# Kernel optimization log

Measured on AMD Instinct MI355X. Metric: run time of the kernel, lower is better.

## Reference

```python
import jax, jax.numpy as jnp
import numpy as np

H = 128          # hidden_size
EF = 2           # expansion_factor
E = H * EF       # expanded hidden size
K = 4            # conv kernel size
R = 8            # dt_rank = ceil(128/16)
L = 2            # num_layers
BATCH = 2
SEQ = 1024
EPS = 1e-5


def rmsnorm(x, w):
    return x * jax.lax.rsqrt(jnp.mean(x * x, axis=-1, keepdims=True) + EPS) * w


def causal_conv1d(x, w, b):
    # x: (b, l, E); w: (E, 1, K) depthwise; left-pad K-1 => causal, output len l
    xt = jnp.transpose(x, (0, 2, 1))  # (b, E, l)
    out = jax.lax.conv_general_dilated(
        xt, w, window_strides=(1,), padding=[(K - 1, 0)],
        dimension_numbers=("NCH", "OIH", "NCH"), feature_group_count=E)
    out = out + b[None, :, None]
    return jnp.transpose(out, (0, 2, 1))


def sscan(xc, delta, A, Bm, Cm, Dp):
    # xc, delta: (b,l,E); A: (E,n); Bm, Cm: (b,l,n); Dp: (E,)
    deltaA = jnp.exp(jnp.einsum('bld,dn->bldn', delta, A))          # (b,l,E,n)
    deltaBx = jnp.einsum('bld,bln,bld->bldn', delta, Bm, xc)        # (b,l,E,n)

    def step(h, inp):
        dA_t, dBx_t, C_t = inp           # (b,E,n), (b,E,n), (b,n)
        h = dA_t * h + dBx_t
        y = jnp.einsum('bdn,bn->bd', h, C_t)
        return h, y

    b = xc.shape[0]
    h0 = jnp.zeros((b, E, A.shape[1]), dtype=xc.dtype)
    _, ys = jax.lax.scan(
        step, h0,
        (jnp.transpose(deltaA, (1, 0, 2, 3)),
         jnp.transpose(deltaBx, (1, 0, 2, 3)),
         jnp.transpose(Cm, (1, 0, 2))))
    y = jnp.transpose(ys, (1, 0, 2))     # (b,l,E)
    return y + Dp * xc


def mamba_block(x, in_w, in_b, out_w, out_b, pl_w, pl_b, dt_w, dt_b,
                conv_w, conv_b, A_log, Dp):
    xz = x @ in_w + in_b                 # (b,l,2E)
    xc, skip = jnp.split(xz, [E], axis=-1)
    xc = jax.nn.silu(causal_conv1d(xc, conv_w, conv_b))
    # ssm
    A = -jnp.exp(A_log)                  # (E,H)
    dbc = xc @ pl_w + pl_b               # (b,l,R+2H)
    delta, Bm, Cm = jnp.split(dbc, [R, R + H], axis=-1)
    delta = jax.nn.softplus(delta @ dt_w + dt_b)   # (b,l,E)
    y = sscan(xc, delta, A, Bm, Cm, Dp)
    y = y * jax.nn.silu(skip)
    return y @ out_w + out_b


def forward(x, in_w, in_b, out_w, out_b, pl_w, pl_b, dt_w, dt_b,
            conv_w, conv_b, A_log, Dp, norm_w, final_norm_w):
    for i in range(L):
        x = mamba_block(rmsnorm(x, norm_w[i]), in_w[i], in_b[i], out_w[i],
                        out_b[i], pl_w[i], pl_b[i], dt_w[i], dt_b[i],
                        conv_w[i], conv_b[i], A_log[i], Dp[i]) + x
    return rmsnorm(x, final_norm_w)


def setup_inputs() -> dict:
    key = jax.random.key(0)
    ks = jax.random.split(key, 12)
    s = 0.02
    x = jax.random.normal(ks[0], (BATCH, SEQ, H), dtype=jnp.float32)
    in_w = jax.random.normal(ks[1], (L, H, 2 * E)) * s
    in_b = jnp.zeros((L, 2 * E))
    out_w = jax.random.normal(ks[2], (L, E, H)) * s
    out_b = jnp.zeros((L, H))
    pl_w = jax.random.normal(ks[3], (L, E, R + 2 * H)) * s
    pl_b = jnp.zeros((L, R + 2 * H))
    dt_w = jax.random.normal(ks[4], (L, R, E)) * s
    dt_b = jnp.zeros((L, E))
    conv_w = jax.random.normal(ks[5], (L, E, 1, K)) * (1.0 / np.sqrt(K))
    conv_b = jnp.zeros((L, E))
    A_log = jnp.broadcast_to(jnp.log(jnp.arange(1, H + 1, dtype=jnp.float32)),
                             (L, E, H))
    Dp = jnp.ones((L, E))
    norm_w = jnp.ones((L, H))
    final_norm_w = jnp.ones((H,))
    return {"x": x, "in_w": in_w, "in_b": in_b, "out_w": out_w,
            "out_b": out_b, "pl_w": pl_w, "pl_b": pl_b, "dt_w": dt_w,
            "dt_b": dt_b, "conv_w": conv_w, "conv_b": conv_b,
            "A_log": A_log, "Dp": Dp, "norm_w": norm_w,
            "final_norm_w": final_norm_w}


def reference(x, in_w, in_b, out_w, out_b, pl_w, pl_b, dt_w, dt_b,
              conv_w, conv_b, A_log, Dp, norm_w, final_norm_w):
    return forward(x, in_w, in_b, out_w, out_b, pl_w, pl_b, dt_w, dt_b,
                   conv_w, conv_b, A_log, Dp, norm_w, final_norm_w)
```

## Files before the change

### kernel.cpp

```cpp
#include <hip/hip_runtime.h>
#include <hip/hip_bf16.h>

#define HH 128
#define EE 256
#define KK 4
#define RR 8
#define LL 2
#define BB 2
#define SS 1024
#define BT (BB*SS)
#define NJ (RR+2*HH)
#define GG 16
#define CH (SS/GG)
#define EPS 1e-5f
#define LOG2E 1.44269504088896f

__device__ __forceinline__ float silu_f(float v) {
    return v / (1.0f + __expf(-v));
}

__global__ __launch_bounds__(256) void k_wdt(
    const float* __restrict__ plw, const float* __restrict__ plb,
    const float* __restrict__ dtw, const float* __restrict__ dtb,
    float* __restrict__ Wdt, float* __restrict__ bdt)
{
    const int l = blockIdx.x >> 2, q = blockIdx.x & 3;
    const int j = threadIdx.x;
    const float* dtwl = dtw + (size_t)l * RR * EE;
    const float* plwl = plw + (size_t)l * EE * NJ;
    float wr[RR];
    #pragma unroll
    for (int r = 0; r < RR; r++) wr[r] = dtwl[r * EE + j];
    float* Wl = Wdt + (size_t)l * EE * EE;
    for (int e = q * 64; e < q * 64 + 64; e++) {
        float a = 0.0f;
        #pragma unroll
        for (int r = 0; r < RR; r++) a += plwl[(size_t)e * NJ + r] * wr[r];
        Wl[(size_t)e * EE + j] = a;
    }
    if (q == 0) {
        float a = dtb[l * EE + j];
        #pragma unroll
        for (int r = 0; r < RR; r++) a += plb[l * NJ + r] * wr[r];
        bdt[l * EE + j] = a;
    }
}

__global__ __launch_bounds__(512) void k_front(
    const float* __restrict__ resin, const float* __restrict__ inw,
    const float* __restrict__ inb, const float* __restrict__ nw,
    const float* __restrict__ cw, const float* __restrict__ cb,
    const float* __restrict__ plw, const float* __restrict__ plb,
    const float* __restrict__ Wdt, const float* __restrict__ bdt,
    float* __restrict__ zbuf, float* __restrict__ xcT,
    float* __restrict__ BC4, float* __restrict__ deltaT,
    float* __restrict__ sT)
{
    __shared__ float xn[11][132];
    __shared__ float xci[11][256];
    __shared__ float xcb[8][256];
    const int bt0 = blockIdx.x * 8;
    const int tid = threadIdx.x;
    const int lb = ((bt0 & (SS - 1)) == 0) ? 0 : 3;
    {
        const int tt = tid >> 5, lane = tid & 31;
        if (tt < lb + 8) {
            const int bt = bt0 - lb + tt;
            const float4 xv = *(const float4*)(resin + (size_t)bt * HH + lane * 4);
            float ss = xv.x*xv.x + xv.y*xv.y + xv.z*xv.z + xv.w*xv.w;
            ss += __shfl_xor(ss, 16); ss += __shfl_xor(ss, 8);
            ss += __shfl_xor(ss, 4);  ss += __shfl_xor(ss, 2);
            ss += __shfl_xor(ss, 1);
            const float rs = rsqrtf(ss * (1.0f / HH) + EPS);
            const float4 wv = *(const float4*)(nw + lane * 4);
            xn[tt][lane*4+0] = xv.x * rs * wv.x;
            xn[tt][lane*4+1] = xv.y * rs * wv.y;
            xn[tt][lane*4+2] = xv.z * rs * wv.z;
            xn[tt][lane*4+3] = xv.w * rs * wv.w;
        }
    }
    __syncthreads();
    if (tid < 256) {
        const int j = tid;
        float acc[11];
        const float bj = inb[j];
        #pragma unroll
        for (int t = 0; t < 11; t++) acc[t] = bj;
        float w0n = inw[0*512 + j], w1n = inw[1*512 + j];
        float w2n = inw[2*512 + j], w3n = inw[3*512 + j];
        for (int k4 = 0; k4 < 32; k4++) {
            const float w0 = w0n, w1 = w1n, w2 = w2n, w3 = w3n;
            if (k4 < 31) {
                const int k = (k4 + 1) * 4;
                w0n = inw[(k+0)*512 + j]; w1n = inw[(k+1)*512 + j];
                w2n = inw[(k+2)*512 + j]; w3n = inw[(k+3)*512 + j];
            }
            const int k = k4 * 4;
            #pragma unroll
            for (int t = 0; t < 11; t++) {
                const float4 xv = *(const float4*)(&xn[t][k]);
                acc[t] += w0*xv.x + w1*xv.y + w2*xv.z + w3*xv.w;
            }
        }
        #pragma unroll
        for (int t = 0; t < 11; t++)
            if (t < lb + 8) xci[t][j] = acc[t];
    } else {
        const int j = tid - 256;
        float acc[8];
        const float bj = inb[256 + j];
        #pragma unroll
        for (int t = 0; t < 8; t++) acc[t] = bj;
        float w0n = inw[0*512 + 256 + j], w1n = inw[1*512 + 256 + j];
        float w2n = inw[2*512 + 256 + j], w3n = inw[3*512 + 256 + j];
        for (int k4 = 0; k4 < 32; k4++) {
            const float w0 = w0n, w1 = w1n, w2 = w2n, w3 = w3n;
            if (k4 < 31) {
                const int k = (k4 + 1) * 4;
                w0n = inw[(k+0)*512 + 256 + j]; w1n = inw[(k+1)*512 + 256 + j];
                w2n = inw[(k+2)*512 + 256 + j]; w3n = inw[(k+3)*512 + 256 + j];
            }
            const int k = k4 * 4;
            #pragma unroll
            for (int t = 0; t < 8; t++) {
                const float4 xv = *(const float4*)(&xn[lb + t][k]);
                acc[t] += w0*xv.x + w1*xv.y + w2*xv.z + w3*xv.w;
            }
        }
        #pragma unroll
        for (int t = 0; t < 8; t++)
            zbuf[(size_t)(bt0 + t) * 256 + j] = acc[t];
    }
    __syncthreads();
    {
        const int e = tid & 255, hf = tid >> 8;
        const float w0 = cw[e*4+0], w1 = cw[e*4+1], w2 = cw[e*4+2], w3 = cw[e*4+3];
        const float bias = cb[e];
        float xcv[4];
        #pragma unroll
        for (int i = 0; i < 4; i++) {
            const int m = lb + hf * 4 + i;
            const float a0  = xci[m][e];
            const float am1 = (m >= 1) ? xci[m-1][e] : 0.0f;
            const float am2 = (m >= 2) ? xci[m-2][e] : 0.0f;
            const float am3 = (m >= 3) ? xci[m-3][e] : 0.0f;
            const float v = bias + w3*a0 + w2*am1 + w1*am2 + w0*am3;
            const float o = silu_f(v);
            xcv[i] = o;
            xcb[hf*4 + i][e] = o;
        }
        *(float4*)(xcT + (size_t)e * BT + bt0 + hf * 4) =
            make_float4(xcv[0], xcv[1], xcv[2], xcv[3]);
    }
    __syncthreads();
    const int j = tid & 255, path = tid >> 8;
    if (path == 0) {
        const int nn = j & 127, isC = j >> 7;
        const float* wp = plw + RR + isC * HH + nn;
        float acc[8];
        const float bj = plb[RR + isC * HH + nn];
        #pragma unroll
        for (int t = 0; t < 8; t++) acc[t] = bj;
        float w0n = wp[0*NJ], w1n = wp[1*NJ], w2n = wp[2*NJ], w3n = wp[3*NJ];
        for (int e4 = 0; e4 < 64; e4++) {
            const float w0 = w0n, w1 = w1n, w2 = w2n, w3 = w3n;
            if (e4 < 63) {
                const int e = (e4 + 1) * 4;
                w0n = wp[(size_t)(e+0)*NJ]; w1n = wp[(size_t)(e+1)*NJ];
                w2n = wp[(size_t)(e+2)*NJ]; w3n = wp[(size_t)(e+3)*NJ];
            }
            const int e = e4 * 4;
            #pragma unroll
            for (int t = 0; t < 8; t++) {
                const float4 xv = *(const float4*)(&xcb[t][e]);
                acc[t] += w0*xv.x + w1*xv.y + w2*xv.z + w3*xv.w;
            }
        }
        const int tq0 = bt0 >> 2;
        float* p0 = BC4 + ((size_t)tq0 * 128 + nn) * 8 + isC * 4;
        *(float4*)p0 = make_float4(acc[0], acc[1], acc[2], acc[3]);
        float* p1 = BC4 + ((size_t)(tq0 + 1) * 128 + nn) * 8 + isC * 4;
        *(float4*)p1 = make_float4(acc[4], acc[5], acc[6], acc[7]);
    } else {
        const float* wp = Wdt + j;
        float acc[8];
        const float bj = bdt[j];
        #pragma unroll
        for (int t = 0; t < 8; t++) acc[t] = bj;
        float w0n = wp[0*EE], w1n = wp[1*EE], w2n = wp[2*EE], w3n = wp[3*EE];
        for (int e4 = 0; e4 < 64; e4++) {
            const float w0 = w0n, w1 = w1n, w2 = w2n, w3 = w3n;
            if (e4 < 63) {
                const int e = (e4 + 1) * 4;
                w0n = wp[(size_t)(e+0)*EE]; w1n = wp[(size_t)(e+1)*EE];
                w2n = wp[(size_t)(e+2)*EE]; w3n = wp[(size_t)(e+3)*EE];
            }
            const int e = e4 * 4;
            #pragma unroll
            for (int t = 0; t < 8; t++) {
                const float4 xv = *(const float4*)(&xcb[t][e]);
                acc[t] += w0*xv.x + w1*xv.y + w2*xv.z + w3*xv.w;
            }
        }
        float spv[8], sv[8];
        #pragma unroll
        for (int t = 0; t < 8; t++) {
            const float d = acc[t];
            const float sp = (d > 15.0f) ? d : log1pf(__expf(d));
            spv[t] = sp;
            sv[t] = sp * xcb[t][j];
        }
        float* drp = deltaT + (size_t)j * BT + bt0;
        *(float4*)(drp)     = make_float4(spv[0], spv[1], spv[2], spv[3]);
        *(float4*)(drp + 4) = make_float4(spv[4], spv[5], spv[6], spv[7]);
        float* srp = sT + (size_t)j * BT + bt0;
        *(float4*)(srp)     = make_float4(sv[0], sv[1], sv[2], sv[3]);
        *(float4*)(srp + 4) = make_float4(sv[4], sv[5], sv[6], sv[7]);
    }
}

__global__ __launch_bounds__(128, 4) void k_scan_local(
    const float* __restrict__ BC4, const float* __restrict__ deltaT,
    const float* __restrict__ sT, const float* __restrict__ Alog,
    float* __restrict__ yT, float* __restrict__ hchain,
    float* __restrict__ dsum)
{
    __shared__ float part[4][16][68];
    __shared__ float ybuf[4][CH];
    const int blk = blockIdx.x;
    const int wgid = (blk & 7) * 256 + (blk >> 3);
    const int eq = wgid & 63;
    const int r0 = wgid >> 6;
    const int b = r0 >> 4;
    const int g = r0 & 15;
    const int e0 = eq * 4;
    const int n = threadIdx.x;
    const int t0 = g * CH;

    float An[4], h[4], cum[4];
    #pragma unroll
    for (int ee = 0; ee < 4; ee++) {
        An[ee] = -__expf(Alog[(e0 + ee) * HH + n]) * LOG2E;
        h[ee] = 0.0f; cum[ee] = 0.0f;
    }
    const float* bc = BC4 + ((size_t)((b * 256 + g * 16) * 128 + n)) * 8;
    const float* dr[4]; const float* sr[4];
    #pragma unroll
    for (int ee = 0; ee < 4; ee++) {
        dr[ee] = deltaT + (size_t)(e0 + ee) * BT + b * SS + t0;
        sr[ee] = sT + (size_t)(e0 + ee) * BT + b * SS + t0;
    }
    float4 pB = *(const float4*)(bc);
    float4 pC = *(const float4*)(bc + 4);
    float4 pd[4], ps[4];
    #pragma unroll
    for (int ee = 0; ee < 4; ee++) {
        pd[ee] = *(const float4*)dr[ee];
        ps[ee] = *(const float4*)sr[ee];
    }
    const int tl = n >> 3, jj = n & 7;
    for (int sc = 0; sc < 4; sc++) {
        #pragma unroll
        for (int q = 0; q < 4; q++) {
            const int qq = sc * 4 + q;
            const float4 cB = pB, cC = pC;
            float4 cd[4], cs[4];
            #pragma unroll
            for (int ee = 0; ee < 4; ee++) { cd[ee] = pd[ee]; cs[ee] = ps[ee]; }
            if (qq < 15) {
                const size_t off = (size_t)(qq + 1) * 1024;
                pB = *(const float4*)(bc + off);
                pC = *(const float4*)(bc + off + 4);
                const int t = (qq + 1) * 4;
                #pragma unroll
                for (int ee = 0; ee < 4; ee++) {
                    pd[ee] = *(const float4*)(dr[ee] + t);
                    ps[ee] = *(const float4*)(sr[ee] + t);
                }
            }
            #pragma unroll
            for (int ee = 0; ee < 4; ee++) {
                float a;
                a = exp2f(cd[ee].x*An[ee]); h[ee] = a*h[ee] + cs[ee].x*cB.x;
                part[ee][q*4+0][n] = h[ee]*cC.x;
                a = exp2f(cd[ee].y*An[ee]); h[ee] = a*h[ee] + cs[ee].y*cB.y;
                part[ee][q*4+1][n] = h[ee]*cC.y;
                a = exp2f(cd[ee].z*An[ee]); h[ee] = a*h[ee] + cs[ee].z*cB.z;
                part[ee][q*4+2][n] = h[ee]*cC.z;
                a = exp2f(cd[ee].w*An[ee]); h[ee] = a*h[ee] + cs[ee].w*cB.w;
                part[ee][q*4+3][n] = h[ee]*cC.w;
                cum[ee] += (cd[ee].x + cd[ee].y) + (cd[ee].z + cd[ee].w);
            }
        }
        __syncthreads();
        #pragma unroll
        for (int ee = 0; ee < 4; ee++) {
            float s0 = 0, s1 = 0, s2 = 0, s3 = 0;
            #pragma unroll
            for (int i = 0; i < 4; i++) {
                const float4 p = *(const float4*)(&part[ee][tl][jj*16 + i*4]);
                s0 += p.x; s1 += p.y; s2 += p.z; s3 += p.w;
            }
            float r = (s0 + s1) + (s2 + s3);
            r += __shfl_xor(r, 1); r += __shfl_xor(r, 2); r += __shfl_xor(r, 4);
            if (jj == 0) ybuf[ee][sc*16 + tl] = r;
        }
        __syncthreads();
    }
    {
        const int ee = n >> 5, tt = n & 31;
        float* yp = yT + (size_t)(e0 + ee) * BT + b * SS + t0;
        yp[tt] = ybuf[ee][tt];
        yp[tt + 32] = ybuf[ee][tt + 32];
    }
    #pragma unroll
    for (int ee = 0; ee < 4; ee++)
        hchain[(size_t)(((b * EE + e0 + ee) * GG) + g) * 128 + n] = h[ee];
    if (n == 0) {
        #pragma unroll
        for (int ee = 0; ee < 4; ee++)
            dsum[(b * EE + e0 + ee) * GG + g] = cum[ee];
    }
}

__global__ __launch_bounds__(128, 4) void k_scan_fix(
    const float* __restrict__ BC4, const float* __restrict__ deltaT,
    const float* __restrict__ Alog, const float* __restrict__ hchain,
    const float* __restrict__ dsum, float* __restrict__ yT)
{
    __shared__ float part[4][16][68];
    __shared__ float ybuf[4][CH];
    const int blk = blockIdx.x;
    const int wgid = (blk & 7) * 240 + (blk >> 3);
    const int eq = wgid & 63;
    const int r0 = wgid >> 6;
    const int b = r0 / 15;
    const int g = 1 + (r0 % 15);
    const int e0 = eq * 4;
    const int n = threadIdx.x;
    const int t0 = g * CH;

    float An[4], w[4], D[4];
    #pragma unroll
    for (int ee = 0; ee < 4; ee++) {
        An[ee] = -__expf(Alog[(e0 + ee) * HH + n]) * LOG2E;
        w[ee] = 0.0f; D[ee] = 0.0f;
    }
    {
        for (int gp = 0; gp < g; gp++) {
            #pragma unroll
            for (int ee = 0; ee < 4; ee++) {
                const float he = hchain[(size_t)(((b * EE + e0 + ee) * GG) + gp) * 128 + n];
                const float ds = dsum[(b * EE + e0 + ee) * GG + gp];
                w[ee] = exp2f(An[ee] * ds) * w[ee] + he;
            }
        }
    }
    const float* bc = BC4 + ((size_t)((b * 256 + g * 16) * 128 + n)) * 8;
    const float* dr[4];
    #pragma unroll
    for (int ee = 0; ee < 4; ee++)
        dr[ee] = deltaT + (size_t)(e0 + ee) * BT + b * SS + t0;

    float4 pC = *(const float4*)(bc + 4);
    float4 pd[4];
    #pragma unroll
    for (int ee = 0; ee < 4; ee++) pd[ee] = *(const float4*)dr[ee];

    const int tl = n >> 3, jj = n & 7;
    for (int sc = 0; sc < 4; sc++) {
        #pragma unroll
        for (int q = 0; q < 4; q++) {
            const int qq = sc * 4 + q;
            const float4 cC = pC;
            float4 cd[4];
            #pragma unroll
            for (int ee = 0; ee < 4; ee++) cd[ee] = pd[ee];
            if (qq < 15) {
                const size_t off = (size_t)(qq + 1) * 1024;
                pC = *(const float4*)(bc + off + 4);
                const int t = (qq + 1) * 4;
                #pragma unroll
                for (int ee = 0; ee < 4; ee++)
                    pd[ee] = *(const float4*)(dr[ee] + t);
            }
            #pragma unroll
            for (int ee = 0; ee < 4; ee++) {
                D[ee] += cd[ee].x; part[ee][q*4+0][n] = exp2f(An[ee]*D[ee]) * w[ee] * cC.x;
                D[ee] += cd[ee].y; part[ee][q*4+1][n] = exp2f(An[ee]*D[ee]) * w[ee] * cC.y;
                D[ee] += cd[ee].z; part[ee][q*4+2][n] = exp2f(An[ee]*D[ee]) * w[ee] * cC.z;
                D[ee] += cd[ee].w; part[ee][q*4+3][n] = exp2f(An[ee]*D[ee]) * w[ee] * cC.w;
            }
        }
        __syncthreads();
        #pragma unroll
        for (int ee = 0; ee < 4; ee++) {
            float s0 = 0, s1 = 0, s2 = 0, s3 = 0;
            #pragma unroll
            for (int i = 0; i < 4; i++) {
                const float4 p = *(const float4*)(&part[ee][tl][jj*16 + i*4]);
                s0 += p.x; s1 += p.y; s2 += p.z; s3 += p.w;
            }
            float r = (s0 + s1) + (s2 + s3);
            r += __shfl_xor(r, 1); r += __shfl_xor(r, 2); r += __shfl_xor(r, 4);
            if (jj == 0) ybuf[ee][sc*16 + tl] = r;
        }
        __syncthreads();
    }
    {
        const int ee = n >> 5, tt = n & 31;
        float* yp = yT + (size_t)(e0 + ee) * BT + b * SS + t0;
        yp[tt] += ybuf[ee][tt];
        yp[tt + 32] += ybuf[ee][tt + 32];
    }
}

__global__ __launch_bounds__(256) void k_gate(
    const float* __restrict__ yT, const float* __restrict__ xcT,
    const float* __restrict__ zbuf, const float* __restrict__ Dp,
    const float* __restrict__ ow, const float* __restrict__ ob,
    const float* __restrict__ resin, float* __restrict__ xres)
{
    __shared__ float gs[8][256];
    __shared__ float p2[8][128];
    const int bt0 = blockIdx.x * 8;
    const int tid = threadIdx.x;
    {
        const int e = tid;
        const float dp = Dp[e];
        const float* yp = yT + (size_t)e * BT + bt0;
        const float* xp = xcT + (size_t)e * BT + bt0;
        #pragma unroll
        for (int tq = 0; tq < 2; tq++) {
            const float4 y4 = *(const float4*)(yp + tq * 4);
            const float4 x4 = *(const float4*)(xp + tq * 4);
            float sk;
            sk = zbuf[(size_t)(bt0 + tq*4 + 0) * 256 + e];
            gs[tq*4+0][e] = (y4.x + dp * x4.x) * silu_f(sk);
            sk = zbuf[(size_t)(bt0 + tq*4 + 1) * 256 + e];
            gs[tq*4+1][e] = (y4.y + dp * x4.y) * silu_f(sk);
            sk = zbuf[(size_t)(bt0 + tq*4 + 2) * 256 + e];
            gs[tq*4+2][e] = (y4.z + dp * x4.z) * silu_f(sk);
            sk = zbuf[(size_t)(bt0 + tq*4 + 3) * 256 + e];
            gs[tq*4+3][e] = (y4.w + dp * x4.w) * silu_f(sk);
        }
    }
    __syncthreads();
    const int j = tid & 127;
    const int kh = tid >> 7;
    float acc[8];
    #pragma unroll
    for (int t = 0; t < 8; t++) acc[t] = 0.0f;
    const int eb = kh * 128;
    float w0n = ow[(eb+0)*HH + j], w1n = ow[(eb+1)*HH + j];
    float w2n = ow[(eb+2)*HH + j], w3n = ow[(eb+3)*HH + j];
    for (int e4 = 0; e4 < 32; e4++) {
        const float w0 = w0n, w1 = w1n, w2 = w2n, w3 = w3n;
        if (e4 < 31) {
            const int e = eb + (e4 + 1) * 4;
            w0n = ow[(e+0)*HH + j]; w1n = ow[(e+1)*HH + j];
            w2n = ow[(e+2)*HH + j]; w3n = ow[(e+3)*HH + j];
        }
        const int e = eb + e4 * 4;
        #pragma unroll
        for (int t = 0; t < 8; t++) {
            const float4 g4 = *(const float4*)(&gs[t][e]);
            acc[t] += w0*g4.x + w1*g4.y + w2*g4.z + w3*g4.w;
        }
    }
    if (kh == 1) {
        #pragma unroll
        for (int t = 0; t < 8; t++) p2[t][j] = acc[t];
    }
    __syncthreads();
    if (kh == 0) {
        const float bj = ob[j];
        #pragma unroll
        for (int t = 0; t < 8; t++) {
            const float r = acc[t] + p2[t][j] + bj
                          + resin[(size_t)(bt0 + t) * HH + j];
            xres[(size_t)(bt0 + t) * HH + j] = r;
        }
    }
}

__global__ __launch_bounds__(256) void k_gate_final(
    const float* __restrict__ yT, const float* __restrict__ xcT,
    const float* __restrict__ zbuf, const float* __restrict__ Dp,
    const float* __restrict__ ow, const float* __restrict__ ob,
    const float* __restrict__ resin, const float* __restrict__ fw,
    float* __restrict__ out)
{
    __shared__ float gs[8][256];
    __shared__ float p2[8][132];
    const int bt0 = blockIdx.x * 8;
    const int tid = threadIdx.x;
    {
        const int e = tid;
        const float dp = Dp[e];
        const float* yp = yT + (size_t)e * BT + bt0;
        const float* xp = xcT + (size_t)e * BT + bt0;
        #pragma unroll
        for (int tq = 0; tq < 2; tq++) {
            const float4 y4 = *(const float4*)(yp + tq * 4);
            const float4 x4 = *(const float4*)(xp + tq * 4);
            float sk;
            sk = zbuf[(size_t)(bt0 + tq*4 + 0) * 256 + e];
            gs[tq*4+0][e] = (y4.x + dp * x4.x) * silu_f(sk);
            sk = zbuf[(size_t)(bt0 + tq*4 + 1) * 256 + e];
            gs[tq*4+1][e] = (y4.y + dp * x4.y) * silu_f(sk);
            sk = zbuf[(size_t)(bt0 + tq*4 + 2) * 256 + e];
            gs[tq*4+2][e] = (y4.z + dp * x4.z) * silu_f(sk);
            sk = zbuf[(size_t)(bt0 + tq*4 + 3) * 256 + e];
            gs[tq*4+3][e] = (y4.w + dp * x4.w) * silu_f(sk);
        }
    }
    __syncthreads();
    const int j = tid & 127;
    const int kh = tid >> 7;
    {
        float acc[8];
        #pragma unroll
        for (int t = 0; t < 8; t++) acc[t] = 0.0f;
        const int eb = kh * 128;
        float w0n = ow[(eb+0)*HH + j], w1n = ow[(eb+1)*HH + j];
        float w2n = ow[(eb+2)*HH + j], w3n = ow[(eb+3)*HH + j];
        for (int e4 = 0; e4 < 32; e4++) {
            const float w0 = w0n, w1 = w1n, w2 = w2n, w3 = w3n;
            if (e4 < 31) {
                const int e = eb + (e4 + 1) * 4;
                w0n = ow[(e+0)*HH + j]; w1n = ow[(e+1)*HH + j];
                w2n = ow[(e+2)*HH + j]; w3n = ow[(e+3)*HH + j];
            }
            const int e = eb + e4 * 4;
            #pragma unroll
            for (int t = 0; t < 8; t++) {
                const float4 g4 = *(const float4*)(&gs[t][e]);
                acc[t] += w0*g4.x + w1*g4.y + w2*g4.z + w3*g4.w;
            }
        }
        if (kh == 1) {
            #pragma unroll
            for (int t = 0; t < 8; t++) p2[t][j] = acc[t];
        }
        __syncthreads();
        if (kh == 0) {
            const float bj = ob[j];
            #pragma unroll
            for (int t = 0; t < 8; t++) {
                const float r = acc[t] + p2[t][j] + bj
                              + resin[(size_t)(bt0 + t) * HH + j];
                p2[t][j] = r;
            }
        }
    }
    __syncthreads();
    {
        const int t = tid >> 5, lane = tid & 31;
        const float4 v = *(const float4*)(&p2[t][lane * 4]);
        float ss = v.x*v.x + v.y*v.y + v.z*v.z + v.w*v.w;
        ss += __shfl_xor(ss, 16); ss += __shfl_xor(ss, 8);
        ss += __shfl_xor(ss, 4);  ss += __shfl_xor(ss, 2);
        ss += __shfl_xor(ss, 1);
        const float rs = rsqrtf(ss * (1.0f / HH) + EPS);
        const float4 w = *(const float4*)(fw + lane * 4);
        float4 o;
        o.x = v.x * rs * w.x; o.y = v.y * rs * w.y;
        o.z = v.z * rs * w.z; o.w = v.w * rs * w.w;
        *(float4*)(out + (size_t)(bt0 + t) * HH + lane * 4) = o;
    }
}

extern "C" void kernel_launch(void* const* d_in, const int* in_sizes, int n_in,
                              void* d_out, int out_size, void* d_ws, size_t ws_size,
                              hipStream_t stream)
{
    const float* x      = (const float*)d_in[0];
    const float* in_w   = (const float*)d_in[1];
    const float* in_b   = (const float*)d_in[2];
    const float* out_w  = (const float*)d_in[3];
    const float* out_b  = (const float*)d_in[4];
    const float* pl_w   = (const float*)d_in[5];
    const float* pl_b   = (const float*)d_in[6];
    const float* dt_w   = (const float*)d_in[7];
    const float* dt_b   = (const float*)d_in[8];
    const float* conv_w = (const float*)d_in[9];
    const float* conv_b = (const float*)d_in[10];
    const float* A_log  = (const float*)d_in[11];
    const float* Dp     = (const float*)d_in[12];
    const float* norm_w = (const float*)d_in[13];
    const float* fnw    = (const float*)d_in[14];

    float* ws     = (float*)d_ws;
    float* xres   = ws;
    float* zbuf   = xres   + 262144;
    float* xcT    = zbuf   + 524288;
    float* BC4    = xcT    + 524288;
    float* deltaT = BC4    + 524288;
    float* sT     = deltaT + 524288;
    float* yT     = sT     + 524288;
    float* hchain = yT     + 524288;
    float* dsum   = hchain + 1048576;
    float* Wdt    = dsum   + 8192;
    float* bdt    = Wdt    + 131072;

    k_wdt<<<2*4, 256, 0, stream>>>(pl_w, pl_b, dt_w, dt_b, Wdt, bdt);

    for (int l = 0; l < LL; l++) {
        const float* resin = (l == 0) ? x : xres;
        k_front<<<BT/8, 512, 0, stream>>>(
            resin, in_w + (size_t)l*HH*2*EE, in_b + (size_t)l*2*EE,
            norm_w + (size_t)l*HH,
            conv_w + (size_t)l*EE*KK, conv_b + (size_t)l*EE,
            pl_w + (size_t)l*EE*NJ, pl_b + (size_t)l*NJ,
            Wdt + (size_t)l*EE*EE, bdt + (size_t)l*EE,
            zbuf, xcT, BC4, deltaT, sT);
        k_scan_local<<<BB*GG*(EE/4), 128, 0, stream>>>(
            BC4, deltaT, sT, A_log + (size_t)l*EE*HH, yT, hchain, dsum);
        k_scan_fix<<<BB*(GG-1)*(EE/4), 128, 0, stream>>>(
            BC4, deltaT, A_log + (size_t)l*EE*HH, hchain, dsum, yT);
        if (l < LL - 1) {
            k_gate<<<BT/8, 256, 0, stream>>>(
                yT, xcT, zbuf, Dp + (size_t)l*EE,
                out_w + (size_t)l*EE*HH, out_b + (size_t)l*HH, resin, xres);
        } else {
            k_gate_final<<<BT/8, 256, 0, stream>>>(
                yT, xcT, zbuf, Dp + (size_t)l*EE,
                out_w + (size_t)l*EE*HH, out_b + (size_t)l*HH, xres,
                fnw, (float*)d_out);
        }
    }
}
```

Baseline: 237.3 us.

## Restructure chunked scan into state-only pass, combine, and full output pass

Replaces the scan-local plus correction pass with three kernels. The first computes per-chunk end states only, a small combine kernel turns them into carried-in states, and a second full pass starts each chunk from its correct initial state. This removes the correction kernel's per-step exp and prefix loops. It also splits the front kernel into a norm/in-projection kernel writing a full xz buffer and a conv/projection kernel, which drops the redundant halo recomputation. The cost is an extra launch and a second pass over delta, s and B, and -exp(A_log) is now precomputed into a table once per forward.

Result: slower. 244.9 us (+3.2%).

```diff
diff --git a/kernel.cpp b/kernel.cpp
--- a/kernel.cpp
+++ b/kernel.cpp
@@ -19,137 +19,123 @@
     return v / (1.0f + __expf(-v));
 }
 
-__global__ __launch_bounds__(256) void k_wdt(
+__global__ __launch_bounds__(256) void k_prep(
     const float* __restrict__ plw, const float* __restrict__ plb,
     const float* __restrict__ dtw, const float* __restrict__ dtb,
-    float* __restrict__ Wdt, float* __restrict__ bdt)
-{
-    const int l = blockIdx.x >> 2, q = blockIdx.x & 3;
-    const int j = threadIdx.x;
-    const float* dtwl = dtw + (size_t)l * RR * EE;
-    const float* plwl = plw + (size_t)l * EE * NJ;
-    float wr[RR];
-    #pragma unroll
-    for (int r = 0; r < RR; r++) wr[r] = dtwl[r * EE + j];
-    float* Wl = Wdt + (size_t)l * EE * EE;
-    for (int e = q * 64; e < q * 64 + 64; e++) {
-        float a = 0.0f;
-        #pragma unroll
-        for (int r = 0; r < RR; r++) a += plwl[(size_t)e * NJ + r] * wr[r];
-        Wl[(size_t)e * EE + j] = a;
-    }
-    if (q == 0) {
-        float a = dtb[l * EE + j];
-        #pragma unroll
-        for (int r = 0; r < RR; r++) a += plb[l * NJ + r] * wr[r];
-        bdt[l * EE + j] = a;
-    }
-}
-
-__global__ __launch_bounds__(512) void k_front(
-    const float* __restrict__ resin, const float* __restrict__ inw,
+    const float* __restrict__ Alog,
+    float* __restrict__ Wdt, float* __restrict__ bdt,
+    float* __restrict__ Antab)
+{
+    const int blk = blockIdx.x;
+    if (blk < 8) {
+        const int l = blk >> 2, q = blk & 3;
+        const int j = threadIdx.x;
+        const float* dtwl = dtw + (size_t)l * RR * EE;
+        const float* plwl = plw + (size_t)l * EE * NJ;
+        float wr[RR];
+        #pragma unroll
+        for (int r = 0; r < RR; r++) wr[r] = dtwl[r * EE + j];
+        float* Wl = Wdt + (size_t)l * EE * EE;
+        for (int e = q * 64; e < q * 64 + 64; e++) {
+            float a = 0.0f;
+            #pragma unroll
+            for (int r = 0; r < RR; r++) a += plwl[(size_t)e * NJ + r] * wr[r];
+            Wl[(size_t)e * EE + j] = a;
+        }
+        if (q == 0) {
+            float a = dtb[l * EE + j];
+            #pragma unroll
+            for (int r = 0; r < RR; r++) a += plb[l * NJ + r] * wr[r];
+            bdt[l * EE + j] = a;
+        }
+    } else {
+        const int blk2 = blk - 8;
+        const int l = blk2 >> 2, q = blk2 & 3;
+        const size_t base = (size_t)l * EE * HH;
+        for (int i = 0; i < 32; i++) {
+            const int flat = q * 8192 + i * 256 + threadIdx.x;
+            Antab[base + flat] = -__expf(Alog[base + flat]) * LOG2E;
+        }
+    }
+}
+
+__global__ __launch_bounds__(512) void k_norm_inproj(
+    const float* __restrict__ xin, const float* __restrict__ inw,
     const float* __restrict__ inb, const float* __restrict__ nw,
-    const float* __restrict__ cw, const float* __restrict__ cb,
-    const float* __restrict__ plw, const float* __restrict__ plb,
-    const float* __restrict__ Wdt, const float* __restrict__ bdt,
-    float* __restrict__ zbuf, float* __restrict__ xcT,
-    float* __restrict__ BC4, float* __restrict__ deltaT,
-    float* __restrict__ sT)
-{
-    __shared__ float xn[11][132];
-    __shared__ float xci[11][256];
+    float* __restrict__ xz)
+{
+    __shared__ float xn[8][128];
+    const int bt0 = blockIdx.x * 8;
+    const int tid = threadIdx.x;
+    {
+        const int t = tid >> 6, lane = tid & 63;
+        const float2 xv = *(const float2*)(xin + (size_t)(bt0 + t) * HH + lane * 2);
+        float ss = xv.x*xv.x + xv.y*xv.y;
+        #pragma unroll
+        for (int m = 32; m >= 1; m >>= 1) ss += __shfl_xor(ss, m);
+        const float rs = rsqrtf(ss * (1.0f / HH) + EPS);
+        const float2 wv = *(const float2*)(nw + lane * 2);
+        xn[t][lane*2+0] = xv.x * rs * wv.x;
+        xn[t][lane*2+1] = xv.y * rs * wv.y;
+    }
+    __syncthreads();
+    const int j = tid;
+    float acc[8];
+    const float bj = inb[j];
+    #pragma unroll
+    for (int t = 0; t < 8; t++) acc[t] = bj;
+    float w0n = inw[0*512 + j], w1n = inw[1*512 + j];
+    float w2n = inw[2*512 + j], w3n = inw[3*512 + j];
+    for (int k4 = 0; k4 < 32; k4++) {
+        const float w0 = w0n, w1 = w1n, w2 = w2n, w3 = w3n;
+        if (k4 < 31) {
+            const int k = (k4 + 1) * 4;
+            w0n = inw[(k+0)*512 + j]; w1n = inw[(k+1)*512 + j];
+            w2n = inw[(k+2)*512 + j]; w3n = inw[(k+3)*512 + j];
+        }
+        const int k = k4 * 4;
+        #pragma unroll
+        for (int t = 0; t < 8; t++) {
+            const float4 xv = *(const float4*)(&xn[t][k]);
+            acc[t] += w0*xv.x + w1*xv.y + w2*xv.z + w3*xv.w;
+        }
+    }
+    #pragma unroll
+    for (int t = 0; t < 8; t++) xz[(size_t)(bt0 + t) * 512 + j] = acc[t];
+}
+
+__global__ __launch_bounds__(512) void k_cbd(
+    const float* __restrict__ xz, const float* __restrict__ cw,
+    const float* __restrict__ cb, const float* __restrict__ plw,
+    const float* __restrict__ plb, const float* __restrict__ Wdt,
+    const float* __restrict__ bdt,
+    float* __restrict__ xcT, float* __restrict__ BC4,
+    float* __restrict__ deltaT, float* __restrict__ sT)
+{
     __shared__ float xcb[8][256];
     const int bt0 = blockIdx.x * 8;
     const int tid = threadIdx.x;
-    const int lb = ((bt0 & (SS - 1)) == 0) ? 0 : 3;
-    {
-        const int tt = tid >> 5, lane = tid & 31;
-        if (tt < lb + 8) {
-            const int bt = bt0 - lb + tt;
-            const float4 xv = *(const float4*)(resin + (size_t)bt * HH + lane * 4);
-            float ss = xv.x*xv.x + xv.y*xv.y + xv.z*xv.z + xv.w*xv.w;
-            ss += __shfl_xor(ss, 16); ss += __shfl_xor(ss, 8);
-            ss += __shfl_xor(ss, 4);  ss += __shfl_xor(ss, 2);
-            ss += __shfl_xor(ss, 1);
-            const float rs = rsqrtf(ss * (1.0f / HH) + EPS);
-            const float4 wv = *(const float4*)(nw + lane * 4);
-            xn[tt][lane*4+0] = xv.x * rs * wv.x;
-            xn[tt][lane*4+1] = xv.y * rs * wv.y;
-            xn[tt][lane*4+2] = xv.z * rs * wv.z;
-            xn[tt][lane*4+3] = xv.w * rs * wv.w;
-        }
-    }
-    __syncthreads();
-    if (tid < 256) {
-        const int j = tid;
-        float acc[11];
-        const float bj = inb[j];
-        #pragma unroll
-        for (int t = 0; t < 11; t++) acc[t] = bj;
-        float w0n = inw[0*512 + j], w1n = inw[1*512 + j];
-        float w2n = inw[2*512 + j], w3n = inw[3*512 + j];
-        for (int k4 = 0; k4 < 32; k4++) {
-            const float w0 = w0n, w1 = w1n, w2 = w2n, w3 = w3n;
-            if (k4 < 31) {
-                const int k = (k4 + 1) * 4;
-                w0n = inw[(k+0)*512 + j]; w1n = inw[(k+1)*512 + j];
-                w2n = inw[(k+2)*512 + j]; w3n = inw[(k+3)*512 + j];
-            }
-            const int k = k4 * 4;
-            #pragma unroll
-            for (int t = 0; t < 11; t++) {
-                const float4 xv = *(const float4*)(&xn[t][k]);
-                acc[t] += w0*xv.x + w1*xv.y + w2*xv.z + w3*xv.w;
-            }
-        }
-        #pragma unroll
-        for (int t = 0; t < 11; t++)
-            if (t < lb + 8) xci[t][j] = acc[t];
-    } else {
-        const int j = tid - 256;
-        float acc[8];
-        const float bj = inb[256 + j];
-        #pragma unroll
-        for (int t = 0; t < 8; t++) acc[t] = bj;
-        float w0n = inw[0*512 + 256 + j], w1n = inw[1*512 + 256 + j];
-        float w2n = inw[2*512 + 256 + j], w3n = inw[3*512 + 256 + j];
-        for (int k4 = 0; k4 < 32; k4++) {
-            const float w0 = w0n, w1 = w1n, w2 = w2n, w3 = w3n;
-            if (k4 < 31) {
-                const int k = (k4 + 1) * 4;
-                w0n = inw[(k+0)*512 + 256 + j]; w1n = inw[(k+1)*512 + 256 + j];
-                w2n = inw[(k+2)*512 + 256 + j]; w3n = inw[(k+3)*512 + 256 + j];
-            }
-            const int k = k4 * 4;
-            #pragma unroll
-            for (int t = 0; t < 8; t++) {
-                const float4 xv = *(const float4*)(&xn[lb + t][k]);
-                acc[t] += w0*xv.x + w1*xv.y + w2*xv.z + w3*xv.w;
-            }
-        }
-        #pragma unroll
-        for (int t = 0; t < 8; t++)
-            zbuf[(size_t)(bt0 + t) * 256 + j] = acc[t];
-    }
-    __syncthreads();
     {
         const int e = tid & 255, hf = tid >> 8;
+        const int ts = bt0 + hf * 4;
         const float w0 = cw[e*4+0], w1 = cw[e*4+1], w2 = cw[e*4+2], w3 = cw[e*4+3];
         const float bias = cb[e];
+        const float* xp = xz + (size_t)ts * 512 + e;
+        const bool first = ((ts & (SS-1)) == 0);
+        float xm3 = first ? 0.0f : xp[-3*512];
+        float xm2 = first ? 0.0f : xp[-2*512];
+        float xm1 = first ? 0.0f : xp[-1*512];
         float xcv[4];
         #pragma unroll
         for (int i = 0; i < 4; i++) {
-            const int m = lb + hf * 4 + i;
-            const float a0  = xci[m][e];
-            const float am1 = (m >= 1) ? xci[m-1][e] : 0.0f;
-            const float am2 = (m >= 2) ? xci[m-2][e] : 0.0f;
-            const float am3 = (m >= 3) ? xci[m-3][e] : 0.0f;
-            const float v = bias + w3*a0 + w2*am1 + w1*am2 + w0*am3;
+            const float x0 = xp[i*512];
+            const float v = bias + w3*x0 + w2*xm1 + w1*xm2 + w0*xm3;
             const float o = silu_f(v);
             xcv[i] = o;
             xcb[hf*4 + i][e] = o;
-        }
-        *(float4*)(xcT + (size_t)e * BT + bt0 + hf * 4) =
+            xm3 = xm2; xm2 = xm1; xm1 = x0;
+        }
+        *(float4*)(xcT + (size_t)e * BT + ts) =
             make_float4(xcv[0], xcv[1], xcv[2], xcv[3]);
     }
     __syncthreads();
@@ -219,11 +205,102 @@
     }
 }
 
-__global__ __launch_bounds__(128, 4) void k_scan_local(
+__global__ __launch_bounds__(128, 4) void k_scanA(
     const float* __restrict__ BC4, const float* __restrict__ deltaT,
-    const float* __restrict__ sT, const float* __restrict__ Alog,
-    float* __restrict__ yT, float* __restrict__ hchain,
-    float* __restrict__ dsum)
+    const float* __restrict__ sT, const float* __restrict__ Antab,
+    float* __restrict__ hchain, float* __restrict__ dsum)
+{
+    const int blk = blockIdx.x;
+    const int wgid = (blk & 7) * 256 + (blk >> 3);
+    const int eq = wgid & 63;
+    const int r0 = wgid >> 6;
+    const int b = r0 >> 4;
+    const int g = r0 & 15;
+    const int e0 = eq * 4;
+    const int n = threadIdx.x;
+    const int t0 = g * CH;
+
+    float An[4], h[4], cum[4];
+    #pragma unroll
+    for (int ee = 0; ee < 4; ee++) {
+        An[ee] = Antab[(e0 + ee) * HH + n];
+        h[ee] = 0.0f; cum[ee] = 0.0f;
+    }
+    const float* bc = BC4 + ((size_t)((b * 256 + g * 16) * 128 + n)) * 8;
+    const float* dr[4]; const float* sr[4];
+    #pragma unroll
+    for (int ee = 0; ee < 4; ee++) {
+        dr[ee] = deltaT + (size_t)(e0 + ee) * BT + b * SS + t0;
+        sr[ee] = sT + (size_t)(e0 + ee) * BT + b * SS + t0;
+    }
+    float4 pB = *(const float4*)(bc);
+    float4 pd[4], ps[4];
+    #pragma unroll
+    for (int ee = 0; ee < 4; ee++) {
+        pd[ee] = *(const float4*)dr[ee];
+        ps[ee] = *(const float4*)sr[ee];
+    }
+    for (int qq = 0; qq < 16; qq++) {
+        const float4 cB = pB;
+        float4 cd[4], cs[4];
+        #pragma unroll
+        for (int ee = 0; ee < 4; ee++) { cd[ee] = pd[ee]; cs[ee] = ps[ee]; }
+        if (qq < 15) {
+            const size_t off = (size_t)(qq + 1) * 1024;
+            pB = *(const float4*)(bc + off);
+            const int t = (qq + 1) * 4;
+            #pragma unroll
+            for (int ee = 0; ee < 4; ee++) {
+                pd[ee] = *(const float4*)(dr[ee] + t);
+                ps[ee] = *(const float4*)(sr[ee] + t);
+            }
+        }
+        #pragma unroll
+        for (int ee = 0; ee < 4; ee++) {
+            float a;
+            a = exp2f(cd[ee].x*An[ee]); h[ee] = a*h[ee] + cs[ee].x*cB.x;
+            a = exp2f(cd[ee].y*An[ee]); h[ee] = a*h[ee] + cs[ee].y*cB.y;
+            a = exp2f(cd[ee].z*An[ee]); h[ee] = a*h[ee] + cs[ee].z*cB.z;
+            a = exp2f(cd[ee].w*An[ee]); h[ee] = a*h[ee] + cs[ee].w*cB.w;
+            cum[ee] += (cd[ee].x + cd[ee].y) + (cd[ee].z + cd[ee].w);
+        }
+    }
+    #pragma unroll
+    for (int ee = 0; ee < 4; ee++)
+        hchain[(size_t)(((b * EE + e0 + ee) * GG) + g) * 128 + n] = h[ee];
+    if (n == 0) {
+        #pragma unroll
+        for (int ee = 0; ee < 4; ee++)
+            dsum[(b * EE + e0 + ee) * GG + g] = cum[ee];
+    }
+}
+
+__global__ __launch_bounds__(128) void k_combine(
+    const float* __restrict__ Antab, const float* __restrict__ dsum,
+    float* __restrict__ hchain)
+{
+    const int be = blockIdx.x;
+    const int e = be & 255;
+    const int n = threadIdx.x;
+    const float An = Antab[e * HH + n];
+    const size_t base = (size_t)be * GG * 128 + n;
+    float he[GG], ds[GG];
+    #pragma unroll
+    for (int g = 0; g < GG; g++) he[g] = hchain[base + (size_t)g * 128];
+    #pragma unroll
+    for (int g = 0; g < GG; g++) ds[g] = dsum[be * GG + g];
+    float h = 0.0f;
+    #pragma unroll
+    for (int g = 0; g < GG; g++) {
+        hchain[base + (size_t)g * 128] = h;
+        h = exp2f(An * ds[g]) * h + he[g];
+    }
+}
+
+__global__ __launch_bounds__(128, 4) void k_scanB(
+    const float* __restrict__ BC4, const float* __restrict__ deltaT,
+    const float* __restrict__ sT, const float* __restrict__ Antab,
+    const float* __restrict__ hchain, float* __restrict__ yT)
 {
     __shared__ float part[4][16][68];
     __shared__ float ybuf[4][CH];
@@ -237,11 +314,11 @@
     const int n = threadIdx.x;
     const int t0 = g * CH;
 
-    float An[4], h[4], cum[4];
+    float An[4], h[4];
     #pragma unroll
     for (int ee = 0; ee < 4; ee++) {
-        An[ee] = -__expf(Alog[(e0 + ee) * HH + n]) * LOG2E;
-        h[ee] = 0.0f; cum[ee] = 0.0f;
+        An[ee] = Antab[(e0 + ee) * HH + n];
+        h[ee] = hchain[(size_t)(((b * EE + e0 + ee) * GG) + g) * 128 + n];
     }
     const float* bc = BC4 + ((size_t)((b * 256 + g * 16) * 128 + n)) * 8;
     const float* dr[4]; const float* sr[4];
@@ -289,7 +366,6 @@
                 part[ee][q*4+2][n] = h[ee]*cC.z;
                 a = exp2f(cd[ee].w*An[ee]); h[ee] = a*h[ee] + cs[ee].w*cB.w;
                 part[ee][q*4+3][n] = h[ee]*cC.w;
-                cum[ee] += (cd[ee].x + cd[ee].y) + (cd[ee].z + cd[ee].w);
             }
         }
         __syncthreads();
@@ -313,111 +389,11 @@
         yp[tt] = ybuf[ee][tt];
         yp[tt + 32] = ybuf[ee][tt + 32];
     }
-    #pragma unroll
-    for (int ee = 0; ee < 4; ee++)
-        hchain[(size_t)(((b * EE + e0 + ee) * GG) + g) * 128 + n] = h[ee];
-    if (n == 0) {
-        #pragma unroll
-        for (int ee = 0; ee < 4; ee++)
-            dsum[(b * EE + e0 + ee) * GG + g] = cum[ee];
-    }
-}
-
-__global__ __launch_bounds__(128, 4) void k_scan_fix(
-    const float* __restrict__ BC4, const float* __restrict__ deltaT,
-    const float* __restrict__ Alog, const float* __restrict__ hchain,
-    const float* __restrict__ dsum, float* __restrict__ yT)
-{
-    __shared__ float part[4][16][68];
-    __shared__ float ybuf[4][CH];
-    const int blk = blockIdx.x;
-    const int wgid = (blk & 7) * 240 + (blk >> 3);
-    const int eq = wgid & 63;
-    const int r0 = wgid >> 6;
-    const int b = r0 / 15;
-    const int g = 1 + (r0 % 15);
-    const int e0 = eq * 4;
-    const int n = threadIdx.x;
-    const int t0 = g * CH;
-
-    float An[4], w[4], D[4];
-    #pragma unroll
-    for (int ee = 0; ee < 4; ee++) {
-        An[ee] = -__expf(Alog[(e0 + ee) * HH + n]) * LOG2E;
-        w[ee] = 0.0f; D[ee] = 0.0f;
-    }
-    {
-        for (int gp = 0; gp < g; gp++) {
-            #pragma unroll
-            for (int ee = 0; ee < 4; ee++) {
-                const float he = hchain[(size_t)(((b * EE + e0 + ee) * GG) + gp) * 128 + n];
-                const float ds = dsum[(b * EE + e0 + ee) * GG + gp];
-                w[ee] = exp2f(An[ee] * ds) * w[ee] + he;
-            }
-        }
-    }
-    const float* bc = BC4 + ((size_t)((b * 256 + g * 16) * 128 + n)) * 8;
-    const float* dr[4];
-    #pragma unroll
-    for (int ee = 0; ee < 4; ee++)
-        dr[ee] = deltaT + (size_t)(e0 + ee) * BT + b * SS + t0;
-
-    float4 pC = *(const float4*)(bc + 4);
-    float4 pd[4];
-    #pragma unroll
-    for (int ee = 0; ee < 4; ee++) pd[ee] = *(const float4*)dr[ee];
-
-    const int tl = n >> 3, jj = n & 7;
-    for (int sc = 0; sc < 4; sc++) {
-        #pragma unroll
-        for (int q = 0; q < 4; q++) {
-            const int qq = sc * 4 + q;
-            const float4 cC = pC;
-            float4 cd[4];
-            #pragma unroll
-            for (int ee = 0; ee < 4; ee++) cd[ee] = pd[ee];
-            if (qq < 15) {
-                const size_t off = (size_t)(qq + 1) * 1024;
-                pC = *(const float4*)(bc + off + 4);
-                const int t = (qq + 1) * 4;
-                #pragma unroll
-                for (int ee = 0; ee < 4; ee++)
-                    pd[ee] = *(const float4*)(dr[ee] + t);
-            }
-            #pragma unroll
-            for (int ee = 0; ee < 4; ee++) {
-                D[ee] += cd[ee].x; part[ee][q*4+0][n] = exp2f(An[ee]*D[ee]) * w[ee] * cC.x;
-                D[ee] += cd[ee].y; part[ee][q*4+1][n] = exp2f(An[ee]*D[ee]) * w[ee] * cC.y;
-                D[ee] += cd[ee].z; part[ee][q*4+2][n] = exp2f(An[ee]*D[ee]) * w[ee] * cC.z;
-                D[ee] += cd[ee].w; part[ee][q*4+3][n] = exp2f(An[ee]*D[ee]) * w[ee] * cC.w;
-            }
-        }
-        __syncthreads();
-        #pragma unroll
-        for (int ee = 0; ee < 4; ee++) {
-            float s0 = 0, s1 = 0, s2 = 0, s3 = 0;
-            #pragma unroll
-            for (int i = 0; i < 4; i++) {
-                const float4 p = *(const float4*)(&part[ee][tl][jj*16 + i*4]);
-                s0 += p.x; s1 += p.y; s2 += p.z; s3 += p.w;
-            }
-            float r = (s0 + s1) + (s2 + s3);
-            r += __shfl_xor(r, 1); r += __shfl_xor(r, 2); r += __shfl_xor(r, 4);
-            if (jj == 0) ybuf[ee][sc*16 + tl] = r;
-        }
-        __syncthreads();
-    }
-    {
-        const int ee = n >> 5, tt = n & 31;
-        float* yp = yT + (size_t)(e0 + ee) * BT + b * SS + t0;
-        yp[tt] += ybuf[ee][tt];
-        yp[tt + 32] += ybuf[ee][tt + 32];
-    }
 }
 
 __global__ __launch_bounds__(256) void k_gate(
     const float* __restrict__ yT, const float* __restrict__ xcT,
-    const float* __restrict__ zbuf, const float* __restrict__ Dp,
+    const float* __restrict__ xz, const float* __restrict__ Dp,
     const float* __restrict__ ow, const float* __restrict__ ob,
     const float* __restrict__ resin, float* __restrict__ xres)
 {
@@ -435,13 +411,13 @@
             const float4 y4 = *(const float4*)(yp + tq * 4);
             const float4 x4 = *(const float4*)(xp + tq * 4);
             float sk;
-            sk = zbuf[(size_t)(bt0 + tq*4 + 0) * 256 + e];
+            sk = xz[(size_t)(bt0 + tq*4 + 0) * 512 + 256 + e];
             gs[tq*4+0][e] = (y4.x + dp * x4.x) * silu_f(sk);
-            sk = zbuf[(size_t)(bt0 + tq*4 + 1) * 256 + e];
+            sk = xz[(size_t)(bt0 + tq*4 + 1) * 512 + 256 + e];
             gs[tq*4+1][e] = (y4.y + dp * x4.y) * silu_f(sk);
-            sk = zbuf[(size_t)(bt0 + tq*4 + 2) * 256 + e];
+            sk = xz[(size_t)(bt0 + tq*4 + 2) * 512 + 256 + e];
             gs[tq*4+2][e] = (y4.z + dp * x4.z) * silu_f(sk);
-            sk = zbuf[(size_t)(bt0 + tq*4 + 3) * 256 + e];
+            sk = xz[(size_t)(bt0 + tq*4 + 3) * 512 + 256 + e];
             gs[tq*4+3][e] = (y4.w + dp * x4.w) * silu_f(sk);
         }
     }
@@ -486,7 +462,7 @@
 
 __global__ __launch_bounds__(256) void k_gate_final(
     const float* __restrict__ yT, const float* __restrict__ xcT,
-    const float* __restrict__ zbuf, const float* __restrict__ Dp,
+    const float* __restrict__ xz, const float* __restrict__ Dp,
     const float* __restrict__ ow, const float* __restrict__ ob,
     const float* __restrict__ resin, const float* __restrict__ fw,
     float* __restrict__ out)
@@ -505,13 +481,13 @@
             const float4 y4 = *(const float4*)(yp + tq * 4);
             const float4 x4 = *(const float4*)(xp + tq * 4);
             float sk;
-            sk = zbuf[(size_t)(bt0 + tq*4 + 0) * 256 + e];
+            sk = xz[(size_t)(bt0 + tq*4 + 0) * 512 + 256 + e];
             gs[tq*4+0][e] = (y4.x + dp * x4.x) * silu_f(sk);
-            sk = zbuf[(size_t)(bt0 + tq*4 + 1) * 256 + e];
+            sk = xz[(size_t)(bt0 + tq*4 + 1) * 512 + 256 + e];
             gs[tq*4+1][e] = (y4.y + dp * x4.y) * silu_f(sk);
-            sk = zbuf[(size_t)(bt0 + tq*4 + 2) * 256 + e];
+            sk = xz[(size_t)(bt0 + tq*4 + 2) * 512 + 256 + e];
             gs[tq*4+2][e] = (y4.z + dp * x4.z) * silu_f(sk);
-            sk = zbuf[(size_t)(bt0 + tq*4 + 3) * 256 + e];
+            sk = xz[(size_t)(bt0 + tq*4 + 3) * 512 + 256 + e];
             gs[tq*4+3][e] = (y4.w + dp * x4.w) * silu_f(sk);
         }
     }
@@ -593,8 +569,8 @@
 
     float* ws     = (float*)d_ws;
     float* xres   = ws;
-    float* zbuf   = xres   + 262144;
-    float* xcT    = zbuf   + 524288;
+    float* xz     = xres   + 262144;
+    float* xcT    = xz     + 1048576;
     float* BC4    = xcT    + 524288;
     float* deltaT = BC4    + 524288;
     float* sT     = deltaT + 524288;
@@ -603,29 +579,34 @@
     float* dsum   = hchain + 1048576;
     float* Wdt    = dsum   + 8192;
     float* bdt    = Wdt    + 131072;
-
-    k_wdt<<<2*4, 256, 0, stream>>>(pl_w, pl_b, dt_w, dt_b, Wdt, bdt);
+    float* Antab  = bdt    + 512;
+
+    k_prep<<<16, 256, 0, stream>>>(pl_w, pl_b, dt_w, dt_b, A_log,
+                                   Wdt, bdt, Antab);
 
     for (int l = 0; l < LL; l++) {
         const float* resin = (l == 0) ? x : xres;
-        k_front<<<BT/8, 512, 0, stream>>>(
+        k_norm_inproj<<<BT/8, 512, 0, stream>>>(
             resin, in_w + (size_t)l*HH*2*EE, in_b + (size_t)l*2*EE,
-            norm_w + (size_t)l*HH,
-            conv_w + (size_t)l*EE*KK, conv_b + (size_t)l*EE,
+            norm_w + (size_t)l*HH, xz);
+        k_cbd<<<BT/8, 512, 0, stream>>>(
+            xz, conv_w + (size_t)l*EE*KK, conv_b + (size_t)l*EE,
             pl_w + (size_t)l*EE*NJ, pl_b + (size_t)l*NJ,
             Wdt + (size_t)l*EE*EE, bdt + (size_t)l*EE,
-            zbuf, xcT, BC4, deltaT, sT);
-        k_scan_local<<<BB*GG*(EE/4), 128, 0, stream>>>(
-            BC4, deltaT, sT, A_log + (size_t)l*EE*HH, yT, hchain, dsum);
-        k_scan_fix<<<BB*(GG-1)*(EE/4), 128, 0, stream>>>(
-            BC4, deltaT, A_log + (size_t)l*EE*HH, hchain, dsum, yT);
+            xcT, BC4, deltaT, sT);
+        k_scanA<<<BB*GG*(EE/4), 128, 0, stream>>>(
+            BC4, deltaT, sT, Antab + (size_t)l*EE*HH, hchain, dsum);
+        k_combine<<<BB*EE, 128, 0, stream>>>(
+            Antab + (size_t)l*EE*HH, dsum, hchain);
+        k_scanB<<<BB*GG*(EE/4), 128, 0, stream>>>(
+            BC4, deltaT, sT, Antab + (size_t)l*EE*HH, hchain, yT);
         if (l < LL - 1) {
             k_gate<<<BT/8, 256, 0, stream>>>(
-                yT, xcT, zbuf, Dp + (size_t)l*EE,
+                yT, xcT, xz, Dp + (size_t)l*EE,
                 out_w + (size_t)l*EE*HH, out_b + (size_t)l*HH, resin, xres);
         } else {
             k_gate_final<<<BT/8, 256, 0, stream>>>(
-                yT, xcT, zbuf, Dp + (size_t)l*EE,
+                yT, xcT, xz, Dp + (size_t)l*EE,
                 out_w + (size_t)l*EE*HH, out_b + (size_t)l*HH, xres,
                 fnw, (float*)d_out);
         }
```
